# Kernel tuning notes

Measured on AMD Instinct MI355X. Metric: run time of the kernel, lower is better.

## Reference

```python
import jax, jax.numpy as jnp
import numpy as np

ALPHA = 1.0


def setup_inputs() -> dict:
    key = jax.random.key(0)
    k1, k2 = jax.random.split(key)
    B, T, N, L = 512, 50, 6400, 10
    spikes = jax.random.uniform(k1, (B, T, N), dtype=jnp.float32)
    labels = jax.random.randint(k2, (B,), 0, L, dtype=jnp.int64)
    rates = jnp.zeros((N, L), dtype=jnp.float32)
    return {"spikes": spikes, "labels": labels, "rates": rates, "n_labels": L}


def reference(spikes, labels, rates, n_labels):
    # spikes: [B, T, N]; labels: [B]; rates: [N, L]
    s = spikes.sum(axis=1)  # [B, N] spike counts per sample
    # segment-sum over batch keyed by label (replaces per-label nonzero+gather loop)
    seg_sum = jax.ops.segment_sum(s, labels, num_segments=n_labels)          # [L, N]
    counts = jax.ops.segment_sum(jnp.ones(labels.shape, s.dtype), labels,
                                 num_segments=n_labels)                       # [L]
    mean = seg_sum / jnp.maximum(counts, 1.0)[:, None]                        # [L, N]
    # original only updates column i when that label is present in the batch
    rates_new = jnp.where(counts[None, :] > 0, ALPHA * rates + mean.T, rates)  # [N, L]
    assignments = jnp.argmax(rates_new, axis=1)                               # [N]
    return assignments, rates_new
```

## Files before the change

### kernel.cpp

```cpp
#include <hip/hip_runtime.h>
#include <math.h>


template <typename A>
__global__ void zero_ws_k(A* __restrict__ seg, int* __restrict__ counts,
                          int segN, int L) {
    int i = blockIdx.x * blockDim.x + threadIdx.x;
    if (i < segN) seg[i] = (A)0;
    if (i < L) counts[i] = 0;
}

__global__ void count_k(const int* __restrict__ labels, int* __restrict__ counts,
                        int B) {
    int b = blockIdx.x * blockDim.x + threadIdx.x;
    if (b < B) atomicAdd(&counts[labels[b]], 1);
}

template <typename A>
__global__ void accum4_k(const float* __restrict__ spikes,
                         const int* __restrict__ labels,
                         A* __restrict__ seg, int T, int N) {
    const int b = blockIdx.y;
    const int v = blockIdx.x * blockDim.x + threadIdx.x;
    const int V = N >> 2;
    if (v >= V) return;
    const float4* p = (const float4*)(spikes + (size_t)b * T * N) + v;
    A s0 = 0, s1 = 0, s2 = 0, s3 = 0;
#pragma unroll 5
    for (int t = 0; t < T; ++t) {
        float4 x = p[(size_t)t * V];
        s0 += (A)x.x; s1 += (A)x.y; s2 += (A)x.z; s3 += (A)x.w;
    }
    const int l = labels[b];
    A* dst = seg + (size_t)l * N + (size_t)v * 4;
    atomicAdd(dst + 0, s0);
    atomicAdd(dst + 1, s1);
    atomicAdd(dst + 2, s2);
    atomicAdd(dst + 3, s3);
}

template <typename A>
__global__ void accum1_k(const float* __restrict__ spikes,
                         const int* __restrict__ labels,
                         A* __restrict__ seg, int T, int N) {
    const int b = blockIdx.y;
    const int n = blockIdx.x * blockDim.x + threadIdx.x;
    if (n >= N) return;
    const float* p = spikes + (size_t)b * T * N + n;
    A s = 0;
    for (int t = 0; t < T; ++t) s += (A)p[(size_t)t * N];
    atomicAdd(seg + (size_t)labels[b] * N + n, s);
}

template <typename A>
__global__ void finalize_k(const A* __restrict__ seg, const int* __restrict__ counts,
                           const float* __restrict__ rates, float* __restrict__ out,
                           int N, int L, float alpha) {
    int n = blockIdx.x * blockDim.x + threadIdx.x;
    if (n >= N) return;
    float best = -INFINITY;
    int bi = 0;
    for (int l = 0; l < L; ++l) {
        float r = rates[(size_t)n * L + l];
        int c = counts[l];
        float v = (c > 0) ? (alpha * r + (float)(seg[(size_t)l * N + n] / (A)c)) : r;
        out[(size_t)N + (size_t)n * L + l] = v;
        if (v > best) { best = v; bi = l; }
    }
    out[n] = (float)bi;
}

template <typename A>
static void run_path(const float* spikes, const int* labels, const float* rates,
                     float* out, void* d_ws, int B, int T, int N, int L,
                     hipStream_t stream) {
    const int segN = L * N;
    A* seg = (A*)d_ws;
    int* counts = (int*)((char*)d_ws + (size_t)segN * sizeof(A));

    int zthreads = 256;
    int zblocks = (segN + zthreads - 1) / zthreads;
    zero_ws_k<A><<<dim3(zblocks), dim3(zthreads), 0, stream>>>(seg, counts, segN, L);

    count_k<<<dim3((B + 255) / 256), dim3(256), 0, stream>>>(labels, counts, B);

    if ((N & 3) == 0) {
        const int V = N >> 2;
        const int th = 320;
        dim3 g((V + th - 1) / th, B);
        accum4_k<A><<<g, dim3(th), 0, stream>>>(spikes, labels, seg, T, N);
    } else {
        dim3 g((N + 255) / 256, B);
        accum1_k<A><<<g, dim3(256), 0, stream>>>(spikes, labels, seg, T, N);
    }

    finalize_k<A><<<dim3((N + 255) / 256), dim3(256), 0, stream>>>(
        seg, counts, rates, out, N, L, 1.0f);
}

extern "C" void kernel_launch(void* const* d_in, const int* in_sizes, int n_in,
                              void* d_out, int out_size, void* d_ws, size_t ws_size,
                              hipStream_t stream) {
    const float* spikes = (const float*)d_in[0];
    const int*   labels = (const int*)d_in[1];
    const float* rates  = (const float*)d_in[2];
    const int L = 10;
    const int B = in_sizes[1];
    const int N = in_sizes[2] / L;
    const int T = in_sizes[0] / (B * N);
    float* out = (float*)d_out;

    const size_t needD = (size_t)L * N * sizeof(double) + 64;
    if (ws_size >= needD) {
        run_path<double>(spikes, labels, rates, out, d_ws, B, T, N, L, stream);
    } else {
        run_path<float>(spikes, labels, rates, out, d_ws, B, T, N, L, stream);
    }
}
```

Before: 847.3 us.

## Replace atomic segment-sum with per-group register partials and fused finalize

Each block handles a group of batch rows and accumulates per-label sums in registers via predicated selects, writing partials to workspace instead of issuing global double atomics. The finalize kernel reduces partials in double, computes label counts in shared memory, and emits rates and argmax, removing the zero and count launches. This targets atomic contention, at the cost of extra workspace traffic for partials and float rather than double accumulation within each group.

```diff
diff --git a/kernel.cpp b/kernel.cpp
--- a/kernel.cpp
+++ b/kernel.cpp
@@ -2,100 +2,99 @@
 #include <math.h>
 
 
-template <typename A>
-__global__ void zero_ws_k(A* __restrict__ seg, int* __restrict__ counts,
-                          int segN, int L) {
-    int i = blockIdx.x * blockDim.x + threadIdx.x;
-    if (i < segN) seg[i] = (A)0;
-    if (i < L) counts[i] = 0;
+#define L_FIXED 10
+
+__global__ void __launch_bounds__(64) partial2_k(
+    const float* __restrict__ spikes, const int* __restrict__ labels,
+    float* __restrict__ part, int B, int T, int N, int GB) {
+    const int g = blockIdx.y;
+    const int v = blockIdx.x * blockDim.x + threadIdx.x;
+    const int V = N >> 1;
+    if (v >= V) return;
+
+    float a0[L_FIXED], a1[L_FIXED];
+#pragma unroll
+    for (int l = 0; l < L_FIXED; ++l) { a0[l] = 0.f; a1[l] = 0.f; }
+
+    const int b0 = g * GB;
+    const int b1 = (b0 + GB < B) ? (b0 + GB) : B;
+    for (int b = b0; b < b1; ++b) {
+        const float2* p = (const float2*)(spikes + (size_t)b * T * N) + v;
+        float s0 = 0.f, s1 = 0.f;
+#pragma unroll 10
+        for (int t = 0; t < T; ++t) {
+            float2 x = p[(size_t)t * V];
+            s0 += x.x; s1 += x.y;
+        }
+        const int lab = labels[b];
+#pragma unroll
+        for (int l = 0; l < L_FIXED; ++l)
+            if (lab == l) { a0[l] += s0; a1[l] += s1; }
+    }
+
+    float* dst = part + (size_t)g * L_FIXED * N;
+#pragma unroll
+    for (int l = 0; l < L_FIXED; ++l) {
+        ((float2*)(dst + (size_t)l * N))[v] = make_float2(a0[l], a1[l]);
+    }
 }
 
-__global__ void count_k(const int* __restrict__ labels, int* __restrict__ counts,
-                        int B) {
-    int b = blockIdx.x * blockDim.x + threadIdx.x;
-    if (b < B) atomicAdd(&counts[labels[b]], 1);
+__global__ void __launch_bounds__(64) partial1_k(
+    const float* __restrict__ spikes, const int* __restrict__ labels,
+    float* __restrict__ part, int B, int T, int N, int GB) {
+    const int g = blockIdx.y;
+    const int n = blockIdx.x * blockDim.x + threadIdx.x;
+    if (n >= N) return;
+
+    float a[L_FIXED];
+#pragma unroll
+    for (int l = 0; l < L_FIXED; ++l) a[l] = 0.f;
+
+    const int b0 = g * GB;
+    const int b1 = (b0 + GB < B) ? (b0 + GB) : B;
+    for (int b = b0; b < b1; ++b) {
+        const float* p = spikes + (size_t)b * T * N + n;
+        float s = 0.f;
+#pragma unroll 10
+        for (int t = 0; t < T; ++t) s += p[(size_t)t * N];
+        const int lab = labels[b];
+#pragma unroll
+        for (int l = 0; l < L_FIXED; ++l)
+            if (lab == l) a[l] += s;
+    }
+    float* dst = part + (size_t)g * L_FIXED * N;
+#pragma unroll
+    for (int l = 0; l < L_FIXED; ++l) dst[(size_t)l * N + n] = a[l];
 }
 
-template <typename A>
-__global__ void accum4_k(const float* __restrict__ spikes,
-                         const int* __restrict__ labels,
-                         A* __restrict__ seg, int T, int N) {
-    const int b = blockIdx.y;
-    const int v = blockIdx.x * blockDim.x + threadIdx.x;
-    const int V = N >> 2;
-    if (v >= V) return;
-    const float4* p = (const float4*)(spikes + (size_t)b * T * N) + v;
-    A s0 = 0, s1 = 0, s2 = 0, s3 = 0;
-#pragma unroll 5
-    for (int t = 0; t < T; ++t) {
-        float4 x = p[(size_t)t * V];
-        s0 += (A)x.x; s1 += (A)x.y; s2 += (A)x.z; s3 += (A)x.w;
-    }
-    const int l = labels[b];
-    A* dst = seg + (size_t)l * N + (size_t)v * 4;
-    atomicAdd(dst + 0, s0);
-    atomicAdd(dst + 1, s1);
-    atomicAdd(dst + 2, s2);
-    atomicAdd(dst + 3, s3);
-}
+__global__ void __launch_bounds__(256) finalize_k(
+    const float* __restrict__ part, const int* __restrict__ labels,
+    const float* __restrict__ rates, float* __restrict__ out,
+    int B, int N, int NG, float alpha) {
+    __shared__ int cnt[L_FIXED];
+    if (threadIdx.x < L_FIXED) cnt[threadIdx.x] = 0;
+    __syncthreads();
+    for (int b = threadIdx.x; b < B; b += blockDim.x)
+        atomicAdd(&cnt[labels[b]], 1);
+    __syncthreads();
 
-template <typename A>
-__global__ void accum1_k(const float* __restrict__ spikes,
-                         const int* __restrict__ labels,
-                         A* __restrict__ seg, int T, int N) {
-    const int b = blockIdx.y;
     const int n = blockIdx.x * blockDim.x + threadIdx.x;
     if (n >= N) return;
-    const float* p = spikes + (size_t)b * T * N + n;
-    A s = 0;
-    for (int t = 0; t < T; ++t) s += (A)p[(size_t)t * N];
-    atomicAdd(seg + (size_t)labels[b] * N + n, s);
-}
 
-template <typename A>
-__global__ void finalize_k(const A* __restrict__ seg, const int* __restrict__ counts,
-                           const float* __restrict__ rates, float* __restrict__ out,
-                           int N, int L, float alpha) {
-    int n = blockIdx.x * blockDim.x + threadIdx.x;
-    if (n >= N) return;
     float best = -INFINITY;
     int bi = 0;
-    for (int l = 0; l < L; ++l) {
-        float r = rates[(size_t)n * L + l];
-        int c = counts[l];
-        float v = (c > 0) ? (alpha * r + (float)(seg[(size_t)l * N + n] / (A)c)) : r;
-        out[(size_t)N + (size_t)n * L + l] = v;
+#pragma unroll
+    for (int l = 0; l < L_FIXED; ++l) {
+        double s = 0.0;
+        for (int g = 0; g < NG; ++g)
+            s += (double)part[((size_t)g * L_FIXED + l) * N + n];
+        const int c = cnt[l];
+        const float r = rates[(size_t)n * L_FIXED + l];
+        const float v = (c > 0) ? (alpha * r + (float)(s / (double)c)) : r;
+        out[(size_t)N + (size_t)n * L_FIXED + l] = v;
         if (v > best) { best = v; bi = l; }
     }
     out[n] = (float)bi;
-}
-
-template <typename A>
-static void run_path(const float* spikes, const int* labels, const float* rates,
-                     float* out, void* d_ws, int B, int T, int N, int L,
-                     hipStream_t stream) {
-    const int segN = L * N;
-    A* seg = (A*)d_ws;
-    int* counts = (int*)((char*)d_ws + (size_t)segN * sizeof(A));
-
-    int zthreads = 256;
-    int zblocks = (segN + zthreads - 1) / zthreads;
-    zero_ws_k<A><<<dim3(zblocks), dim3(zthreads), 0, stream>>>(seg, counts, segN, L);
-
-    count_k<<<dim3((B + 255) / 256), dim3(256), 0, stream>>>(labels, counts, B);
-
-    if ((N & 3) == 0) {
-        const int V = N >> 2;
-        const int th = 320;
-        dim3 g((V + th - 1) / th, B);
-        accum4_k<A><<<g, dim3(th), 0, stream>>>(spikes, labels, seg, T, N);
-    } else {
-        dim3 g((N + 255) / 256, B);
-        accum1_k<A><<<g, dim3(256), 0, stream>>>(spikes, labels, seg, T, N);
-    }
-
-    finalize_k<A><<<dim3((N + 255) / 256), dim3(256), 0, stream>>>(
-        seg, counts, rates, out, N, L, 1.0f);
 }
 
 extern "C" void kernel_launch(void* const* d_in, const int* in_sizes, int n_in,
@@ -104,16 +103,29 @@
     const float* spikes = (const float*)d_in[0];
     const int*   labels = (const int*)d_in[1];
     const float* rates  = (const float*)d_in[2];
-    const int L = 10;
+    const int L = L_FIXED;
     const int B = in_sizes[1];
     const int N = in_sizes[2] / L;
     const int T = in_sizes[0] / (B * N);
     float* out = (float*)d_out;
 
-    const size_t needD = (size_t)L * N * sizeof(double) + 64;
-    if (ws_size >= needD) {
-        run_path<double>(spikes, labels, rates, out, d_ws, B, T, N, L, stream);
+    const size_t per = (size_t)L * N * sizeof(float);
+    int NG = 64;
+    if (per > 0 && (size_t)NG * per > ws_size) NG = (int)(ws_size / per);
+    if (NG < 1) NG = 1;
+    if (NG > B) NG = B;
+    const int GB = (B + NG - 1) / NG;
+    float* part = (float*)d_ws;
+
+    if ((N & 1) == 0) {
+        const int V = N >> 1;
+        dim3 g((V + 63) / 64, NG);
+        partial2_k<<<g, dim3(64), 0, stream>>>(spikes, labels, part, B, T, N, GB);
     } else {
-        run_path<float>(spikes, labels, rates, out, d_ws, B, T, N, L, stream);
+        dim3 g((N + 63) / 64, NG);
+        partial1_k<<<g, dim3(64), 0, stream>>>(spikes, labels, part, B, T, N, GB);
     }
+
+    finalize_k<<<dim3((N + 255) / 256), dim3(256), 0, stream>>>(
+        part, labels, rates, out, B, N, NG, 1.0f);
 }
```

New measurement: 987.9 us. 1.17x slower.
